# Kernel tuning notes

Measured on AMD Instinct MI355X. Metric: run time of the kernel, lower is better.

The kernel has to match this reference:

```python
import jax, jax.numpy as jnp
import numpy as np

B, N, F_IN = 4, 8000, 3          # batch, electrons per event, (x,y,z) features
HID, S, T = 128, 1024, 1024      # MLP hidden, n_sensors, waveform_ticks
INV_SQRT_2PI = 0.3989422804


def _mlp(x, W1, b1, W2, b2):
    h = jax.nn.relu(x @ W1 + b1)
    return h @ W2 + b2


def setup_inputs() -> dict:
    key = jax.random.key(0)
    ks = jax.random.split(key, 12)
    simulator_input = jax.random.normal(ks[0], (B, N, F_IN), dtype=jnp.float32)
    # z positions in tick units, spread across the waveform
    z_positions = jax.random.uniform(ks[1], (B, N), dtype=jnp.float32) * (T - 1)
    mask = jnp.ones((B, N, 1), dtype=jnp.float32)
    s1 = 1.0 / np.sqrt(F_IN)
    s2 = 1.0 / np.sqrt(HID)
    Wp1 = jax.random.normal(ks[2], (F_IN, HID), dtype=jnp.float32) * s1
    bp1 = jnp.zeros((HID,), dtype=jnp.float32)
    Wp2 = jax.random.normal(ks[3], (HID, S), dtype=jnp.float32) * s2
    bp2 = jnp.zeros((S,), dtype=jnp.float32)
    Wa1 = jax.random.normal(ks[4], (F_IN, HID), dtype=jnp.float32) * s1
    ba1 = jnp.zeros((HID,), dtype=jnp.float32)
    Wa2 = jax.random.normal(ks[5], (HID, S), dtype=jnp.float32) * s2
    ba2 = jnp.zeros((S,), dtype=jnp.float32)
    nn_bin_sigma = 5.0 * jnp.ones((1,), dtype=jnp.float32)  # self.variable init
    return dict(simulator_input=simulator_input, z_positions=z_positions, mask=mask,
                Wp1=Wp1, bp1=bp1, Wp2=Wp2, bp2=bp2,
                Wa1=Wa1, ba1=ba1, Wa2=Wa2, ba2=ba2,
                nn_bin_sigma=nn_bin_sigma)


def reference(simulator_input, z_positions, mask,
              Wp1, bp1, Wp2, bp2, Wa1, ba1, Wa2, ba2, nn_bin_sigma):
    # sensor response per electron: sigmoid(prob MLP) * amp MLP * mask  -> [B,N,S]
    sensor_probs = jax.nn.sigmoid(_mlp(simulator_input, Wp1, bp1, Wp2, bp2))
    el_light_amp = _mlp(simulator_input, Wa1, ba1, Wa2, ba2)
    response_of_sensors = el_light_amp * sensor_probs * mask

    # Gaussian binning kernel over waveform ticks: [B,N,T]
    ticks = jnp.arange(T, dtype=simulator_input.dtype)          # linspace(0, T-1, T)
    sigma = nn_bin_sigma[0]
    diff = ticks[None, None, :] - z_positions[:, :, None]
    exp_values = jnp.exp(-(diff ** 2) / (2.0 * sigma ** 2)) * (INV_SQRT_2PI / jnp.sqrt(sigma ** 2))

    # per-batch waveforms = sensor_response.T @ exp_values -> [B,S,T]; then sum over batch
    waveforms = jnp.einsum('bns,bnt->st', response_of_sensors, exp_values)
    return waveforms  # [S, T]
```

## Files before the change

kernel.cpp:

```cpp
#include <hip/hip_runtime.h>


#define BN_E   32000
#define NBLK   125
#define HIDW   128
#define S_DIM  1024
#define T_DIM  1024
#define NBKT   16
#define KSPL   4
#define MAXPAD (BN_E + NBKT * 31)
#define MAXCG  ((MAXPAD + 31) / 32)
#define INV_SQRT_2PI 0.3989422804f

typedef __attribute__((ext_vector_type(8))) unsigned short u16x8;
typedef __attribute__((ext_vector_type(8))) __bf16         bf16x8;
typedef __attribute__((ext_vector_type(4))) float          f32x4;

static __device__ __forceinline__ unsigned short f2bf(float f) {
    union { float f; unsigned int u; } v; v.f = f;
    unsigned int r = v.u + 0x7FFFu + ((v.u >> 16) & 1u);
    return (unsigned short)(r >> 16);
}

static __device__ __forceinline__ f32x4 mfma16(u16x8 a, u16x8 b, f32x4 c) {
    return __builtin_amdgcn_mfma_f32_16x16x32_bf16(
        __builtin_bit_cast(bf16x8, a), __builtin_bit_cast(bf16x8, b), c, 0, 0, 0);
}

static __device__ __forceinline__ int bucket_of(float z) {
    int b = (int)floorf((z - 31.f) * (1.f / 64.f));
    return min(max(b, 0), NBKT - 1);
}

__global__ __launch_bounds__(256) void k_count(const float* __restrict__ z,
                                               int* __restrict__ bc,
                                               float* __restrict__ out) {
    int bx = blockIdx.x;
    if (bx >= NBLK) {
        int idx = (bx - NBLK) * 256 + threadIdx.x;
        ((f32x4*)out)[idx] = (f32x4){0.f, 0.f, 0.f, 0.f};
        return;
    }
    __shared__ int h[NBKT];
    if (threadIdx.x < NBKT) h[threadIdx.x] = 0;
    __syncthreads();
    int e = bx * 256 + threadIdx.x;
    atomicAdd(&h[bucket_of(z[e])], 1);
    __syncthreads();
    if (threadIdx.x < NBKT) bc[bx * NBKT + threadIdx.x] = h[threadIdx.x];
}

__global__ __launch_bounds__(256) void k_fillscan(const float* __restrict__ z,
                                                  const int* __restrict__ bc,
                                                  int* __restrict__ meta,
                                                  int* __restrict__ list) {
    __shared__ int part[16][16];
    __shared__ int segoff[16][16];
    __shared__ int cntL[NBKT], pstartL[NBKT], baseL[NBKT], h[NBKT];
    int t = threadIdx.x, b = t & 15, seg = t >> 4;
    int v[8]; int sum = 0;
#pragma unroll
    for (int i = 0; i < 8; ++i) {
        int blk = seg * 8 + i;
        v[i] = (blk < NBLK) ? bc[blk * NBKT + b] : 0;
        sum += v[i];
    }
    part[seg][b] = sum;
    if (t < NBKT) h[t] = 0;
    __syncthreads();
    if (t < NBKT) {
        int run = 0;
        for (int s = 0; s < 16; ++s) { segoff[s][t] = run; run += part[s][t]; }
        cntL[t] = run;
    }
    __syncthreads();
    if (t == 0) {
        int s = 0;
        for (int i = 0; i < NBKT; ++i) {
            pstartL[i] = s;
            s += ((cntL[i] + 31) >> 5) << 5;
        }
        if (blockIdx.x == 0) {
            for (int i = 0; i < NBKT; ++i) { meta[i] = cntL[i]; meta[32 + i] = pstartL[i]; }
            meta[48] = s;
        }
    }
    __syncthreads();
    if (t < NBKT) {
        int me = blockIdx.x;
        int run = segoff[me >> 3][t];
        for (int k = 0; k < (me & 7); ++k)
            run += bc[((me >> 3) * 8 + k) * NBKT + t];
        baseL[t] = pstartL[t] + run;
    }
    __syncthreads();
    int e = blockIdx.x * 256 + t;
    int b2 = bucket_of(z[e]);
    int r = atomicAdd(&h[b2], 1);
    list[baseL[b2] + r] = e;
}

__global__ __launch_bounds__(256) void k_prep(
    const float* __restrict__ x, const float* __restrict__ zg,
    const float* __restrict__ maskg, const float* __restrict__ sigp,
    const float* __restrict__ Wp1, const float* __restrict__ bp1,
    const float* __restrict__ Wa1, const float* __restrict__ ba1,
    const float* __restrict__ Wp2, const float* __restrict__ Wa2,
    const int* __restrict__ meta, const int* __restrict__ list,
    unsigned short* __restrict__ HpS, unsigned short* __restrict__ HaS,
    unsigned short* __restrict__ GT,
    unsigned short* __restrict__ WfP, unsigned short* __restrict__ WfA) {
    int bx = blockIdx.x;
    if (bx < MAXCG) {
        int pos0 = bx * 32;
        if (pos0 >= meta[48]) return;
        int b = 15;
        while (meta[32 + b] > pos0) --b;
        int tb = b * 64, cnt = meta[b], pstart = meta[32 + b];
        int tid = threadIdx.x;

        __shared__ float W1L[1024];
        __shared__ float zzL[32], cmL[32];
        if (tid < 96)                        ((float4*)W1L)[tid]              = ((const float4*)Wp1)[tid];
        else if (tid < 128)                  ((float4*)(W1L + 384))[tid - 96] = ((const float4*)bp1)[tid - 96];
        else if (tid < 224)                  ((float4*)(W1L + 512))[tid - 128]= ((const float4*)Wa1)[tid - 128];
        else                                 ((float4*)(W1L + 896))[tid - 224]= ((const float4*)ba1)[tid - 224];
        if (tid < 32) {
            int pos = pos0 + tid;
            bool real = (pos - pstart) < cnt;
            int ev = real ? list[pos] : 0;
            float sigma = sigp[0];
            zzL[tid] = real ? zg[ev] : 0.f;
            cmL[tid] = real ? (INV_SQRT_2PI / sigma) * maskg[ev] : 0.f;
        }
        __syncthreads();

        {
            int e_l = tid >> 3, part = tid & 7;
            int pos = pos0 + e_l;
            bool real = (pos - pstart) < cnt;
            int ev = real ? list[pos] : 0;
            float x0 = 0.f, x1 = 0.f, x2 = 0.f;
            if (real) { x0 = x[ev * 3]; x1 = x[ev * 3 + 1]; x2 = x[ev * 3 + 2]; }
            unsigned short hp[16], ha[16];
#pragma unroll
            for (int i = 0; i < 16; ++i) {
                int j = part * 16 + i;
                float hv = x0 * W1L[j] + x1 * W1L[128 + j] + x2 * W1L[256 + j] + W1L[384 + j];
                float av = x0 * W1L[512 + j] + x1 * W1L[640 + j] + x2 * W1L[768 + j] + W1L[896 + j];
                hp[i] = real ? f2bf(fmaxf(hv, 0.f)) : (unsigned short)0;
                ha[i] = real ? f2bf(fmaxf(av, 0.f)) : (unsigned short)0;
            }
#pragma unroll
            for (int h2 = 0; h2 < 2; ++h2) {
                int k0 = part * 16 + h2 * 8;
                int u = ((k0 >> 5) * 4 + ((k0 >> 3) & 3)) * 32 + e_l;
                *(uint4*)&HpS[(size_t)bx * 4096 + u * 8] = ((uint4*)hp)[h2];
                *(uint4*)&HaS[(size_t)bx * 4096 + u * 8] = ((uint4*)ha)[h2];
            }
        }

        {
            float sigma = sigp[0];
            float nis2 = -1.f / (2.f * sigma * sigma);
#pragma unroll
            for (int uu = 0; uu < 2; ++uu) {
                int u = tid * 2 + uu;
                int n8 = u >> 6, q = (u >> 4) & 3, c = u & 15;
                float tt = (float)(tb + n8 * 16 + c);
                unsigned short g8[8];
#pragma unroll
                for (int j = 0; j < 8; ++j) {
                    int e = q * 8 + j;
                    float d = tt - zzL[e];
                    g8[j] = f2bf(cmL[e] * __expf(d * d * nis2));
                }
                *(uint4*)&GT[(size_t)bx * 4096 + u * 8] = *(uint4*)g8;
            }
        }
    } else {
        int bid = bx - MAXCG;
        const float* src = (bid & 64) ? Wa2 : Wp2;
        unsigned short* dst = (bid & 64) ? WfA : WfP;
        int rem = bid & 63;
        int kq = rem >> 2;
        int s  = (rem & 3) * 256 + threadIdx.x;
        int ks = kq >> 2, q = kq & 3;
        unsigned short fr[8];
#pragma unroll
        for (int j = 0; j < 8; ++j)
            fr[j] = f2bf(src[(ks * 32 + q * 8 + j) * S_DIM + s]);
        ((u16x8*)dst)[kq * S_DIM + s] = *(u16x8*)fr;
    }
}

__global__ __launch_bounds__(256, 4) void k_main(
    const unsigned short* __restrict__ HpS, const unsigned short* __restrict__ HaS,
    const unsigned short* __restrict__ WfP, const unsigned short* __restrict__ WfA,
    const float* __restrict__ bp2, const float* __restrict__ ba2,
    const int* __restrict__ meta, const unsigned short* __restrict__ GT,
    float* __restrict__ out) {

    const int bk     = blockIdx.x / KSPL;
    const int kspl   = blockIdx.x % KSPL;
    const int s0     = blockIdx.y * 64;
    const int tb     = bk * 64;
    const int cnt    = meta[bk];
    const int pstart = meta[32 + bk];
    const int nch    = (cnt + 31) >> 5;
    const int per    = (nch + KSPL - 1) / KSPL;
    const int c0     = kspl * per;
    const int c1     = min(nch, c0 + per);
    if (c0 >= c1) return;

    const int tid = threadIdx.x;
    const int w = tid >> 6, l = tid & 63, q = l >> 4, c = l & 15;

    __shared__ __align__(16) uint4 HpL[512];
    __shared__ __align__(16) uint4 HaL[512];
    __shared__ __align__(16) unsigned short RspL[64 * 40];

    const u16x8* WfPv = (const u16x8*)WfP;
    const u16x8* WfAv = (const u16x8*)WfA;
    const int sg = s0 + w * 16 + c;
    u16x8 wP[4], wA[4];
#pragma unroll
    for (int ks = 0; ks < 4; ++ks) {
        wP[ks] = WfPv[(ks * 4 + q) * S_DIM + sg];
        wA[ks] = WfAv[(ks * 4 + q) * S_DIM + sg];
    }
    const float bp2v = bp2[sg];
    const float ba2v = ba2[sg];

    const f32x4 z4 = { 0.f, 0.f, 0.f, 0.f };
    f32x4 acc2[8];
#pragma unroll
    for (int n8 = 0; n8 < 8; ++n8) acc2[n8] = z4;

    const uint4* Hp4 = (const uint4*)HpS;
    const uint4* Ha4 = (const uint4*)HaS;
    const int cgBase = pstart >> 5;
    const u16x8* StHp = (const u16x8*)HpL;
    const u16x8* StHa = (const u16x8*)HaL;

    size_t cb = (size_t)(cgBase + c0) * 512;
    uint4 p0 = Hp4[cb + tid], p1 = Hp4[cb + 256 + tid];
    uint4 a0 = Ha4[cb + tid], a1 = Ha4[cb + 256 + tid];

    for (int ci = c0; ci < c1; ++ci) {
        __syncthreads();
        HpL[tid] = p0; HpL[256 + tid] = p1;
        HaL[tid] = a0; HaL[256 + tid] = a1;
        __syncthreads();

        int nc = min(ci + 1, c1 - 1);
        cb = (size_t)(cgBase + nc) * 512;
        p0 = Hp4[cb + tid]; p1 = Hp4[cb + 256 + tid];
        a0 = Ha4[cb + tid]; a1 = Ha4[cb + 256 + tid];

        const unsigned short* gt = GT + (size_t)(cgBase + ci) * 4096;
        u16x8 bfr[8];
#pragma unroll
        for (int n8 = 0; n8 < 8; ++n8)
            bfr[n8] = *(const u16x8*)&gt[((n8 * 4 + q) * 16 + c) * 8];

        f32x4 aP[2], aA[2];
#pragma unroll
        for (int m = 0; m < 2; ++m) { aP[m] = z4; aA[m] = z4; }
#pragma unroll
        for (int ks = 0; ks < 4; ++ks) {
            u16x8 hp0 = StHp[(ks * 4 + q) * 32 + c];
            u16x8 hp1 = StHp[(ks * 4 + q) * 32 + c + 16];
            u16x8 ha0 = StHa[(ks * 4 + q) * 32 + c];
            u16x8 ha1 = StHa[(ks * 4 + q) * 32 + c + 16];
            aP[0] = mfma16(hp0, wP[ks], aP[0]);
            aP[1] = mfma16(hp1, wP[ks], aP[1]);
            aA[0] = mfma16(ha0, wA[ks], aA[0]);
            aA[1] = mfma16(ha1, wA[ks], aA[1]);
        }

#pragma unroll
        for (int m = 0; m < 2; ++m) {
            f32x4 p = aP[m], a = aA[m];
            unsigned long long pk = 0;
#pragma unroll
            for (int r = 0; r < 4; ++r) {
                float pr = p[r] + bp2v;
                float ar = a[r] + ba2v;
                float sg2 = __builtin_amdgcn_rcpf(1.f + __expf(-pr));
                pk |= (unsigned long long)f2bf(sg2 * ar) << (16 * r);
            }
            int sl = w * 16 + c;
            int e0 = m * 16 + q * 4;
            *(unsigned long long*)&RspL[sl * 40 + e0] = pk;
        }

        u16x8 afr = *(const u16x8*)&RspL[(w * 16 + c) * 40 + q * 8];
#pragma unroll
        for (int n8 = 0; n8 < 8; ++n8)
            acc2[n8] = mfma16(afr, bfr[n8], acc2[n8]);
    }

#pragma unroll
    for (int n8 = 0; n8 < 8; ++n8) {
        int t = tb + n8 * 16 + c;
        if (t < T_DIM) {
            int srow = s0 + w * 16 + q * 4;
#pragma unroll
            for (int r = 0; r < 4; ++r)
                atomicAdd(&out[(srow + r) * T_DIM + t], acc2[n8][r]);
        }
    }
}


extern "C" void kernel_launch(void* const* d_in, const int* in_sizes, int n_in,
                              void* d_out, int out_size, void* d_ws, size_t ws_size,
                              hipStream_t stream) {
    const float* x    = (const float*)d_in[0];
    const float* zp   = (const float*)d_in[1];
    const float* mask = (const float*)d_in[2];
    const float* Wp1  = (const float*)d_in[3];
    const float* bp1  = (const float*)d_in[4];
    const float* Wp2  = (const float*)d_in[5];
    const float* bp2  = (const float*)d_in[6];
    const float* Wa1  = (const float*)d_in[7];
    const float* ba1  = (const float*)d_in[8];
    const float* Wa2  = (const float*)d_in[9];
    const float* ba2  = (const float*)d_in[10];
    const float* sig  = (const float*)d_in[11];

    char* ws = (char*)d_ws;
    unsigned short* HpS  = (unsigned short*)(ws);
    unsigned short* HaS  = (unsigned short*)(ws + 8323072);
    unsigned short* WfP  = (unsigned short*)(ws + 16646144);
    unsigned short* WfA  = (unsigned short*)(ws + 16908288);
    int*            meta = (int*)(ws + 17170432);
    int*            list = (int*)(ws + 17170688);
    int*            bc   = (int*)(ws + 17300736);
    unsigned short* GT   = (unsigned short*)(ws + 17308736);

    k_count<<<NBLK + 1024, 256, 0, stream>>>(zp, bc, (float*)d_out);
    k_fillscan<<<NBLK, 256, 0, stream>>>(zp, bc, meta, list);
    k_prep<<<MAXCG + 128, 256, 0, stream>>>(x, zp, mask, sig,
                                            Wp1, bp1, Wa1, ba1, Wp2, Wa2,
                                            meta, list, HpS, HaS, GT, WfP, WfA);
    k_main<<<dim3(NBKT * KSPL, 16, 1), 256, 0, stream>>>(
        HpS, HaS, WfP, WfA, bp2, ba2, meta, GT, (float*)d_out);
}
```

Baseline: 153.3 us.

## Replace output atomics with partial-sum buffers and a separate reduce kernel

k_main no longer does atomicAdd into a zeroed output. Each block writes plain stores into one of eight 4 MB partial slabs, chosen by k-split and bucket parity, and a new k_reduce kernel sums the slabs into the output. The zero-fill that k_count used to do is removed. This drops atomic contention and the zero-init pass, but adds about 32 MB of partial writes plus a reduce pass that reads them back, and one more kernel launch. Blocks with no work now also store zeros.

```diff
diff --git a/kernel.cpp b/kernel.cpp
--- a/kernel.cpp
+++ b/kernel.cpp
@@ -33,21 +33,14 @@
 }
 
 __global__ __launch_bounds__(256) void k_count(const float* __restrict__ z,
-                                               int* __restrict__ bc,
-                                               float* __restrict__ out) {
-    int bx = blockIdx.x;
-    if (bx >= NBLK) {
-        int idx = (bx - NBLK) * 256 + threadIdx.x;
-        ((f32x4*)out)[idx] = (f32x4){0.f, 0.f, 0.f, 0.f};
-        return;
-    }
+                                               int* __restrict__ bc) {
     __shared__ int h[NBKT];
     if (threadIdx.x < NBKT) h[threadIdx.x] = 0;
     __syncthreads();
-    int e = bx * 256 + threadIdx.x;
+    int e = blockIdx.x * 256 + threadIdx.x;
     atomicAdd(&h[bucket_of(z[e])], 1);
     __syncthreads();
-    if (threadIdx.x < NBKT) bc[bx * NBKT + threadIdx.x] = h[threadIdx.x];
+    if (threadIdx.x < NBKT) bc[blockIdx.x * NBKT + threadIdx.x] = h[threadIdx.x];
 }
 
 __global__ __launch_bounds__(256) void k_fillscan(const float* __restrict__ z,
@@ -199,7 +192,7 @@
     const unsigned short* __restrict__ WfP, const unsigned short* __restrict__ WfA,
     const float* __restrict__ bp2, const float* __restrict__ ba2,
     const int* __restrict__ meta, const unsigned short* __restrict__ GT,
-    float* __restrict__ out) {
+    float* __restrict__ Acc) {
 
     const int bk     = blockIdx.x / KSPL;
     const int kspl   = blockIdx.x % KSPL;
@@ -211,7 +204,6 @@
     const int per    = (nch + KSPL - 1) / KSPL;
     const int c0     = kspl * per;
     const int c1     = min(nch, c0 + per);
-    if (c0 >= c1) return;
 
     const int tid = threadIdx.x;
     const int w = tid >> 6, l = tid & 63, q = l >> 4, c = l & 15;
@@ -220,87 +212,90 @@
     __shared__ __align__(16) uint4 HaL[512];
     __shared__ __align__(16) unsigned short RspL[64 * 40];
 
-    const u16x8* WfPv = (const u16x8*)WfP;
-    const u16x8* WfAv = (const u16x8*)WfA;
-    const int sg = s0 + w * 16 + c;
-    u16x8 wP[4], wA[4];
-#pragma unroll
-    for (int ks = 0; ks < 4; ++ks) {
-        wP[ks] = WfPv[(ks * 4 + q) * S_DIM + sg];
-        wA[ks] = WfAv[(ks * 4 + q) * S_DIM + sg];
-    }
-    const float bp2v = bp2[sg];
-    const float ba2v = ba2[sg];
-
     const f32x4 z4 = { 0.f, 0.f, 0.f, 0.f };
     f32x4 acc2[8];
 #pragma unroll
     for (int n8 = 0; n8 < 8; ++n8) acc2[n8] = z4;
 
-    const uint4* Hp4 = (const uint4*)HpS;
-    const uint4* Ha4 = (const uint4*)HaS;
-    const int cgBase = pstart >> 5;
-    const u16x8* StHp = (const u16x8*)HpL;
-    const u16x8* StHa = (const u16x8*)HaL;
-
-    size_t cb = (size_t)(cgBase + c0) * 512;
-    uint4 p0 = Hp4[cb + tid], p1 = Hp4[cb + 256 + tid];
-    uint4 a0 = Ha4[cb + tid], a1 = Ha4[cb + 256 + tid];
-
-    for (int ci = c0; ci < c1; ++ci) {
-        __syncthreads();
-        HpL[tid] = p0; HpL[256 + tid] = p1;
-        HaL[tid] = a0; HaL[256 + tid] = a1;
-        __syncthreads();
-
-        int nc = min(ci + 1, c1 - 1);
-        cb = (size_t)(cgBase + nc) * 512;
-        p0 = Hp4[cb + tid]; p1 = Hp4[cb + 256 + tid];
-        a0 = Ha4[cb + tid]; a1 = Ha4[cb + 256 + tid];
-
-        const unsigned short* gt = GT + (size_t)(cgBase + ci) * 4096;
-        u16x8 bfr[8];
-#pragma unroll
-        for (int n8 = 0; n8 < 8; ++n8)
-            bfr[n8] = *(const u16x8*)&gt[((n8 * 4 + q) * 16 + c) * 8];
-
-        f32x4 aP[2], aA[2];
-#pragma unroll
-        for (int m = 0; m < 2; ++m) { aP[m] = z4; aA[m] = z4; }
+    if (c0 < c1) {
+        const u16x8* WfPv = (const u16x8*)WfP;
+        const u16x8* WfAv = (const u16x8*)WfA;
+        const int sg = s0 + w * 16 + c;
+        u16x8 wP[4], wA[4];
 #pragma unroll
         for (int ks = 0; ks < 4; ++ks) {
-            u16x8 hp0 = StHp[(ks * 4 + q) * 32 + c];
-            u16x8 hp1 = StHp[(ks * 4 + q) * 32 + c + 16];
-            u16x8 ha0 = StHa[(ks * 4 + q) * 32 + c];
-            u16x8 ha1 = StHa[(ks * 4 + q) * 32 + c + 16];
-            aP[0] = mfma16(hp0, wP[ks], aP[0]);
-            aP[1] = mfma16(hp1, wP[ks], aP[1]);
-            aA[0] = mfma16(ha0, wA[ks], aA[0]);
-            aA[1] = mfma16(ha1, wA[ks], aA[1]);
-        }
-
-#pragma unroll
-        for (int m = 0; m < 2; ++m) {
-            f32x4 p = aP[m], a = aA[m];
-            unsigned long long pk = 0;
-#pragma unroll
-            for (int r = 0; r < 4; ++r) {
-                float pr = p[r] + bp2v;
-                float ar = a[r] + ba2v;
-                float sg2 = __builtin_amdgcn_rcpf(1.f + __expf(-pr));
-                pk |= (unsigned long long)f2bf(sg2 * ar) << (16 * r);
-            }
-            int sl = w * 16 + c;
-            int e0 = m * 16 + q * 4;
-            *(unsigned long long*)&RspL[sl * 40 + e0] = pk;
-        }
-
-        u16x8 afr = *(const u16x8*)&RspL[(w * 16 + c) * 40 + q * 8];
-#pragma unroll
-        for (int n8 = 0; n8 < 8; ++n8)
-            acc2[n8] = mfma16(afr, bfr[n8], acc2[n8]);
-    }
-
+            wP[ks] = WfPv[(ks * 4 + q) * S_DIM + sg];
+            wA[ks] = WfAv[(ks * 4 + q) * S_DIM + sg];
+        }
+        const float bp2v = bp2[sg];
+        const float ba2v = ba2[sg];
+
+        const uint4* Hp4 = (const uint4*)HpS;
+        const uint4* Ha4 = (const uint4*)HaS;
+        const int cgBase = pstart >> 5;
+        const u16x8* StHp = (const u16x8*)HpL;
+        const u16x8* StHa = (const u16x8*)HaL;
+
+        size_t cb = (size_t)(cgBase + c0) * 512;
+        uint4 p0 = Hp4[cb + tid], p1 = Hp4[cb + 256 + tid];
+        uint4 a0 = Ha4[cb + tid], a1 = Ha4[cb + 256 + tid];
+
+        for (int ci = c0; ci < c1; ++ci) {
+            __syncthreads();
+            HpL[tid] = p0; HpL[256 + tid] = p1;
+            HaL[tid] = a0; HaL[256 + tid] = a1;
+            __syncthreads();
+
+            int nc = min(ci + 1, c1 - 1);
+            cb = (size_t)(cgBase + nc) * 512;
+            p0 = Hp4[cb + tid]; p1 = Hp4[cb + 256 + tid];
+            a0 = Ha4[cb + tid]; a1 = Ha4[cb + 256 + tid];
+
+            const unsigned short* gt = GT + (size_t)(cgBase + ci) * 4096;
+            u16x8 bfr[8];
+#pragma unroll
+            for (int n8 = 0; n8 < 8; ++n8)
+                bfr[n8] = *(const u16x8*)&gt[((n8 * 4 + q) * 16 + c) * 8];
+
+            f32x4 aP[2], aA[2];
+#pragma unroll
+            for (int m = 0; m < 2; ++m) { aP[m] = z4; aA[m] = z4; }
+#pragma unroll
+            for (int ks = 0; ks < 4; ++ks) {
+                u16x8 hp0 = StHp[(ks * 4 + q) * 32 + c];
+                u16x8 hp1 = StHp[(ks * 4 + q) * 32 + c + 16];
+                u16x8 ha0 = StHa[(ks * 4 + q) * 32 + c];
+                u16x8 ha1 = StHa[(ks * 4 + q) * 32 + c + 16];
+                aP[0] = mfma16(hp0, wP[ks], aP[0]);
+                aP[1] = mfma16(hp1, wP[ks], aP[1]);
+                aA[0] = mfma16(ha0, wA[ks], aA[0]);
+                aA[1] = mfma16(ha1, wA[ks], aA[1]);
+            }
+
+#pragma unroll
+            for (int m = 0; m < 2; ++m) {
+                f32x4 p = aP[m], a = aA[m];
+                unsigned long long pk = 0;
+#pragma unroll
+                for (int r = 0; r < 4; ++r) {
+                    float pr = p[r] + bp2v;
+                    float ar = a[r] + ba2v;
+                    float sg2 = __builtin_amdgcn_rcpf(1.f + __expf(-pr));
+                    pk |= (unsigned long long)f2bf(sg2 * ar) << (16 * r);
+                }
+                int sl = w * 16 + c;
+                int e0 = m * 16 + q * 4;
+                *(unsigned long long*)&RspL[sl * 40 + e0] = pk;
+            }
+
+            u16x8 afr = *(const u16x8*)&RspL[(w * 16 + c) * 40 + q * 8];
+#pragma unroll
+            for (int n8 = 0; n8 < 8; ++n8)
+                acc2[n8] = mfma16(afr, bfr[n8], acc2[n8]);
+        }
+    }
+
+    float* dst = Acc + ((size_t)(kspl * 2 + (bk & 1)) << 20);
 #pragma unroll
     for (int n8 = 0; n8 < 8; ++n8) {
         int t = tb + n8 * 16 + c;
@@ -308,9 +303,21 @@
             int srow = s0 + w * 16 + q * 4;
 #pragma unroll
             for (int r = 0; r < 4; ++r)
-                atomicAdd(&out[(srow + r) * T_DIM + t], acc2[n8][r]);
-        }
-    }
+                dst[(srow + r) * T_DIM + t] = acc2[n8][r];
+        }
+    }
+}
+
+__global__ __launch_bounds__(256) void k_reduce(const float* __restrict__ Acc,
+                                                float* __restrict__ out) {
+    int i = blockIdx.x * 256 + threadIdx.x;
+    int t4 = (i & 255) * 4;
+    const f32x4* A = (const f32x4*)Acc;
+    const int SL = 1 << 18;
+    f32x4 s = A[i] + A[2 * SL + i] + A[4 * SL + i] + A[6 * SL + i];
+    if (t4 >= 64)
+        s += A[SL + i] + A[3 * SL + i] + A[5 * SL + i] + A[7 * SL + i];
+    ((f32x4*)out)[i] = s;
 }
 
 
@@ -339,12 +346,14 @@
     int*            list = (int*)(ws + 17170688);
     int*            bc   = (int*)(ws + 17300736);
     unsigned short* GT   = (unsigned short*)(ws + 17308736);
-
-    k_count<<<NBLK + 1024, 256, 0, stream>>>(zp, bc, (float*)d_out);
+    float*          Acc  = (float*)(ws + 25631808);
+
+    k_count<<<NBLK, 256, 0, stream>>>(zp, bc);
     k_fillscan<<<NBLK, 256, 0, stream>>>(zp, bc, meta, list);
     k_prep<<<MAXCG + 128, 256, 0, stream>>>(x, zp, mask, sig,
                                             Wp1, bp1, Wa1, ba1, Wp2, Wa2,
                                             meta, list, HpS, HaS, GT, WfP, WfA);
     k_main<<<dim3(NBKT * KSPL, 16, 1), 256, 0, stream>>>(
-        HpS, HaS, WfP, WfA, bp2, ba2, meta, GT, (float*)d_out);
-}
+        HpS, HaS, WfP, WfA, bp2, ba2, meta, GT, Acc);
+    k_reduce<<<1024, 256, 0, stream>>>(Acc, (float*)d_out);
+}
```

After: 153.9 us. No clear change (+0.4%).

## Fuse count/MLP prep into one kernel and compute Gaussian tiles inside main kernel

Applied to the files above, without the earlier changes.

Merges the bucket-count, first-layer MLP, weight conversion and output zeroing into one pre kernel. The hidden activations are now stored in unsorted event order, and k_main gathers them through the sorted list. The Gaussian binning tile is computed on the fly in k_main into shared memory instead of being precomputed to global memory. This removes one kernel launch and the global write and read of the Gaussian tiles. In exchange, k_main does redundant exp work across its 16 sensor-block y tiles, does indirect gathers, and adds an extra barrier per chunk.

```diff
diff --git a/kernel.cpp b/kernel.cpp
--- a/kernel.cpp
+++ b/kernel.cpp
@@ -9,8 +9,12 @@
 #define NBKT   16
 #define KSPL   4
 #define MAXPAD (BN_E + NBKT * 31)
-#define MAXCG  ((MAXPAD + 31) / 32)
 #define INV_SQRT_2PI 0.3989422804f
+
+#define HB 16000
+#define CB NBLK
+#define WB 128
+#define ZB 1024
 
 typedef __attribute__((ext_vector_type(8))) unsigned short u16x8;
 typedef __attribute__((ext_vector_type(8))) __bf16         bf16x8;
@@ -32,22 +36,48 @@
     return min(max(b, 0), NBKT - 1);
 }
 
-__global__ __launch_bounds__(256) void k_count(const float* __restrict__ z,
-                                               int* __restrict__ bc,
-                                               float* __restrict__ out) {
-    int bx = blockIdx.x;
-    if (bx >= NBLK) {
-        int idx = (bx - NBLK) * 256 + threadIdx.x;
+__global__ __launch_bounds__(256) void k_pre(
+    const float* __restrict__ x, const float* __restrict__ zp,
+    const float* __restrict__ Wp1, const float* __restrict__ bp1,
+    const float* __restrict__ Wa1, const float* __restrict__ ba1,
+    const float* __restrict__ Wp2, const float* __restrict__ Wa2,
+    unsigned short* __restrict__ HpU, unsigned short* __restrict__ HaU,
+    unsigned short* __restrict__ WfP, unsigned short* __restrict__ WfA,
+    int* __restrict__ bc, float* __restrict__ out) {
+    __shared__ int h[NBKT];
+    int bx = blockIdx.x, tid = threadIdx.x;
+    if (bx < HB) {
+        int e = bx * 2 + (tid >> 7);
+        int j = tid & 127;
+        float x0 = x[e * 3 + 0], x1 = x[e * 3 + 1], x2 = x[e * 3 + 2];
+        float hp = x0 * Wp1[j] + x1 * Wp1[HIDW + j] + x2 * Wp1[2 * HIDW + j] + bp1[j];
+        float ha = x0 * Wa1[j] + x1 * Wa1[HIDW + j] + x2 * Wa1[2 * HIDW + j] + ba1[j];
+        HpU[e * HIDW + j] = f2bf(fmaxf(hp, 0.f));
+        HaU[e * HIDW + j] = f2bf(fmaxf(ha, 0.f));
+    } else if (bx < HB + CB) {
+        if (tid < NBKT) h[tid] = 0;
+        __syncthreads();
+        int e = (bx - HB) * 256 + tid;
+        atomicAdd(&h[bucket_of(zp[e])], 1);
+        __syncthreads();
+        if (tid < NBKT) bc[(bx - HB) * NBKT + tid] = h[tid];
+    } else if (bx < HB + CB + WB) {
+        int bid = bx - HB - CB;
+        const float* src = (bid & 64) ? Wa2 : Wp2;
+        unsigned short* dst = (bid & 64) ? WfA : WfP;
+        int rem = bid & 63;
+        int kq = rem >> 2;
+        int s  = (rem & 3) * 256 + tid;
+        int ks = kq >> 2, q = kq & 3;
+        unsigned short fr[8];
+#pragma unroll
+        for (int j = 0; j < 8; ++j)
+            fr[j] = f2bf(src[(ks * 32 + q * 8 + j) * S_DIM + s]);
+        ((u16x8*)dst)[kq * S_DIM + s] = *(u16x8*)fr;
+    } else {
+        int idx = (bx - HB - CB - WB) * 256 + tid;
         ((f32x4*)out)[idx] = (f32x4){0.f, 0.f, 0.f, 0.f};
-        return;
-    }
-    __shared__ int h[NBKT];
-    if (threadIdx.x < NBKT) h[threadIdx.x] = 0;
-    __syncthreads();
-    int e = bx * 256 + threadIdx.x;
-    atomicAdd(&h[bucket_of(z[e])], 1);
-    __syncthreads();
-    if (threadIdx.x < NBKT) bc[bx * NBKT + threadIdx.x] = h[threadIdx.x];
+    }
 }
 
 __global__ __launch_bounds__(256) void k_fillscan(const float* __restrict__ z,
@@ -100,105 +130,13 @@
     list[baseL[b2] + r] = e;
 }
 
-__global__ __launch_bounds__(256) void k_prep(
-    const float* __restrict__ x, const float* __restrict__ zg,
-    const float* __restrict__ maskg, const float* __restrict__ sigp,
-    const float* __restrict__ Wp1, const float* __restrict__ bp1,
-    const float* __restrict__ Wa1, const float* __restrict__ ba1,
-    const float* __restrict__ Wp2, const float* __restrict__ Wa2,
-    const int* __restrict__ meta, const int* __restrict__ list,
-    unsigned short* __restrict__ HpS, unsigned short* __restrict__ HaS,
-    unsigned short* __restrict__ GT,
-    unsigned short* __restrict__ WfP, unsigned short* __restrict__ WfA) {
-    int bx = blockIdx.x;
-    if (bx < MAXCG) {
-        int pos0 = bx * 32;
-        if (pos0 >= meta[48]) return;
-        int b = 15;
-        while (meta[32 + b] > pos0) --b;
-        int tb = b * 64, cnt = meta[b], pstart = meta[32 + b];
-        int tid = threadIdx.x;
-
-        __shared__ float W1L[1024];
-        __shared__ float zzL[32], cmL[32];
-        if (tid < 96)                        ((float4*)W1L)[tid]              = ((const float4*)Wp1)[tid];
-        else if (tid < 128)                  ((float4*)(W1L + 384))[tid - 96] = ((const float4*)bp1)[tid - 96];
-        else if (tid < 224)                  ((float4*)(W1L + 512))[tid - 128]= ((const float4*)Wa1)[tid - 128];
-        else                                 ((float4*)(W1L + 896))[tid - 224]= ((const float4*)ba1)[tid - 224];
-        if (tid < 32) {
-            int pos = pos0 + tid;
-            bool real = (pos - pstart) < cnt;
-            int ev = real ? list[pos] : 0;
-            float sigma = sigp[0];
-            zzL[tid] = real ? zg[ev] : 0.f;
-            cmL[tid] = real ? (INV_SQRT_2PI / sigma) * maskg[ev] : 0.f;
-        }
-        __syncthreads();
-
-        {
-            int e_l = tid >> 3, part = tid & 7;
-            int pos = pos0 + e_l;
-            bool real = (pos - pstart) < cnt;
-            int ev = real ? list[pos] : 0;
-            float x0 = 0.f, x1 = 0.f, x2 = 0.f;
-            if (real) { x0 = x[ev * 3]; x1 = x[ev * 3 + 1]; x2 = x[ev * 3 + 2]; }
-            unsigned short hp[16], ha[16];
-#pragma unroll
-            for (int i = 0; i < 16; ++i) {
-                int j = part * 16 + i;
-                float hv = x0 * W1L[j] + x1 * W1L[128 + j] + x2 * W1L[256 + j] + W1L[384 + j];
-                float av = x0 * W1L[512 + j] + x1 * W1L[640 + j] + x2 * W1L[768 + j] + W1L[896 + j];
-                hp[i] = real ? f2bf(fmaxf(hv, 0.f)) : (unsigned short)0;
-                ha[i] = real ? f2bf(fmaxf(av, 0.f)) : (unsigned short)0;
-            }
-#pragma unroll
-            for (int h2 = 0; h2 < 2; ++h2) {
-                int k0 = part * 16 + h2 * 8;
-                int u = ((k0 >> 5) * 4 + ((k0 >> 3) & 3)) * 32 + e_l;
-                *(uint4*)&HpS[(size_t)bx * 4096 + u * 8] = ((uint4*)hp)[h2];
-                *(uint4*)&HaS[(size_t)bx * 4096 + u * 8] = ((uint4*)ha)[h2];
-            }
-        }
-
-        {
-            float sigma = sigp[0];
-            float nis2 = -1.f / (2.f * sigma * sigma);
-#pragma unroll
-            for (int uu = 0; uu < 2; ++uu) {
-                int u = tid * 2 + uu;
-                int n8 = u >> 6, q = (u >> 4) & 3, c = u & 15;
-                float tt = (float)(tb + n8 * 16 + c);
-                unsigned short g8[8];
-#pragma unroll
-                for (int j = 0; j < 8; ++j) {
-                    int e = q * 8 + j;
-                    float d = tt - zzL[e];
-                    g8[j] = f2bf(cmL[e] * __expf(d * d * nis2));
-                }
-                *(uint4*)&GT[(size_t)bx * 4096 + u * 8] = *(uint4*)g8;
-            }
-        }
-    } else {
-        int bid = bx - MAXCG;
-        const float* src = (bid & 64) ? Wa2 : Wp2;
-        unsigned short* dst = (bid & 64) ? WfA : WfP;
-        int rem = bid & 63;
-        int kq = rem >> 2;
-        int s  = (rem & 3) * 256 + threadIdx.x;
-        int ks = kq >> 2, q = kq & 3;
-        unsigned short fr[8];
-#pragma unroll
-        for (int j = 0; j < 8; ++j)
-            fr[j] = f2bf(src[(ks * 32 + q * 8 + j) * S_DIM + s]);
-        ((u16x8*)dst)[kq * S_DIM + s] = *(u16x8*)fr;
-    }
-}
-
 __global__ __launch_bounds__(256, 4) void k_main(
-    const unsigned short* __restrict__ HpS, const unsigned short* __restrict__ HaS,
+    const unsigned short* __restrict__ HpU, const unsigned short* __restrict__ HaU,
     const unsigned short* __restrict__ WfP, const unsigned short* __restrict__ WfA,
     const float* __restrict__ bp2, const float* __restrict__ ba2,
-    const int* __restrict__ meta, const unsigned short* __restrict__ GT,
+    const float* __restrict__ zp, const float* __restrict__ maskg,
+    const float* __restrict__ sigp,
+    const int* __restrict__ meta, const int* __restrict__ list,
     float* __restrict__ out) {
 
     const int bk     = blockIdx.x / KSPL;
@@ -216,9 +154,11 @@
     const int tid = threadIdx.x;
     const int w = tid >> 6, l = tid & 63, q = l >> 4, c = l & 15;
 
-    __shared__ __align__(16) uint4 HpL[512];
-    __shared__ __align__(16) uint4 HaL[512];
+    __shared__ __align__(16) uint4 HpL[16 * 34];
+    __shared__ __align__(16) uint4 HaL[16 * 34];
+    __shared__ __align__(16) uint4 GL[512];
     __shared__ __align__(16) unsigned short RspL[64 * 40];
+    __shared__ float zzL[32], cmL[32];
 
     const u16x8* WfPv = (const u16x8*)WfP;
     const u16x8* WfAv = (const u16x8*)WfA;
@@ -232,47 +172,81 @@
     const float bp2v = bp2[sg];
     const float ba2v = ba2[sg];
 
+    const float sigma = sigp[0];
+    const float coef  = INV_SQRT_2PI / sigma;
+    const float nis2  = -1.f / (2.f * sigma * sigma);
+
     const f32x4 z4 = { 0.f, 0.f, 0.f, 0.f };
     f32x4 acc2[8];
 #pragma unroll
     for (int n8 = 0; n8 < 8; ++n8) acc2[n8] = z4;
 
-    const uint4* Hp4 = (const uint4*)HpS;
-    const uint4* Ha4 = (const uint4*)HaS;
-    const int cgBase = pstart >> 5;
-    const u16x8* StHp = (const u16x8*)HpL;
-    const u16x8* StHa = (const u16x8*)HaL;
-
-    size_t cb = (size_t)(cgBase + c0) * 512;
-    uint4 p0 = Hp4[cb + tid], p1 = Hp4[cb + 256 + tid];
-    uint4 a0 = Ha4[cb + tid], a1 = Ha4[cb + 256 + tid];
+    const uint4* Hp4 = (const uint4*)HpU;
+    const uint4* Ha4 = (const uint4*)HaU;
+    const u16x8* HpV = (const u16x8*)HpL;
+    const u16x8* HaV = (const u16x8*)HaL;
+    const u16x8* GLv = (const u16x8*)GL;
+
+    const int e_l = tid >> 3, kq0 = tid & 7;
+
+    int evS = (c0 * 32 + e_l < cnt) ? list[pstart + c0 * 32 + e_l] : 0;
+    uint4 p0 = Hp4[evS * 16 + kq0], p1 = Hp4[evS * 16 + kq0 + 8];
+    uint4 a0 = Ha4[evS * 16 + kq0], a1 = Ha4[evS * 16 + kq0 + 8];
+    float zzn = 0.f, cmn = 0.f;
+    if (tid < 32) {
+        bool r2 = (c0 * 32 + tid) < cnt;
+        int ev2 = r2 ? list[pstart + c0 * 32 + tid] : 0;
+        zzn = r2 ? zp[ev2] : 0.f;
+        cmn = r2 ? coef * maskg[ev2] : 0.f;
+    }
 
     for (int ci = c0; ci < c1; ++ci) {
         __syncthreads();
-        HpL[tid] = p0; HpL[256 + tid] = p1;
-        HaL[tid] = a0; HaL[256 + tid] = a1;
-        __syncthreads();
+        HpL[kq0 * 34 + e_l] = p0; HpL[(kq0 + 8) * 34 + e_l] = p1;
+        HaL[kq0 * 34 + e_l] = a0; HaL[(kq0 + 8) * 34 + e_l] = a1;
+        if (tid < 32) { zzL[tid] = zzn; cmL[tid] = cmn; }
+        __syncthreads();
+
+        {
+            int q4 = (tid >> 4) & 3;
+            float zr[8], cr[8];
+#pragma unroll
+            for (int j = 0; j < 8; ++j) { zr[j] = zzL[q4 * 8 + j]; cr[j] = cmL[q4 * 8 + j]; }
+#pragma unroll
+            for (int uu = 0; uu < 2; ++uu) {
+                int u = tid + uu * 256;
+                int n8 = u >> 6, cc = u & 15;
+                float tt = (float)(tb + n8 * 16 + cc);
+                unsigned short g8[8];
+#pragma unroll
+                for (int j = 0; j < 8; ++j) {
+                    float d = tt - zr[j];
+                    g8[j] = f2bf(cr[j] * __expf(d * d * nis2));
+                }
+                GL[u] = *(uint4*)g8;
+            }
+        }
 
         int nc = min(ci + 1, c1 - 1);
-        cb = (size_t)(cgBase + nc) * 512;
-        p0 = Hp4[cb + tid]; p1 = Hp4[cb + 256 + tid];
-        a0 = Ha4[cb + tid]; a1 = Ha4[cb + 256 + tid];
-
-        const unsigned short* gt = GT + (size_t)(cgBase + ci) * 4096;
-        u16x8 bfr[8];
-#pragma unroll
-        for (int n8 = 0; n8 < 8; ++n8)
-            bfr[n8] = *(const u16x8*)&gt[((n8 * 4 + q) * 16 + c) * 8];
+        int evSn = (nc * 32 + e_l < cnt) ? list[pstart + nc * 32 + e_l] : 0;
+        p0 = Hp4[evSn * 16 + kq0]; p1 = Hp4[evSn * 16 + kq0 + 8];
+        a0 = Ha4[evSn * 16 + kq0]; a1 = Ha4[evSn * 16 + kq0 + 8];
+        if (tid < 32) {
+            bool r2 = (nc * 32 + tid) < cnt;
+            int ev2 = r2 ? list[pstart + nc * 32 + tid] : 0;
+            zzn = r2 ? zp[ev2] : 0.f;
+            cmn = r2 ? coef * maskg[ev2] : 0.f;
+        }
 
         f32x4 aP[2], aA[2];
 #pragma unroll
         for (int m = 0; m < 2; ++m) { aP[m] = z4; aA[m] = z4; }
 #pragma unroll
         for (int ks = 0; ks < 4; ++ks) {
-            u16x8 hp0 = StHp[(ks * 4 + q) * 32 + c];
-            u16x8 hp1 = StHp[(ks * 4 + q) * 32 + c + 16];
-            u16x8 ha0 = StHa[(ks * 4 + q) * 32 + c];
-            u16x8 ha1 = StHa[(ks * 4 + q) * 32 + c + 16];
+            u16x8 hp0 = HpV[(ks * 4 + q) * 34 + c];
+            u16x8 hp1 = HpV[(ks * 4 + q) * 34 + c + 16];
+            u16x8 ha0 = HaV[(ks * 4 + q) * 34 + c];
+            u16x8 ha1 = HaV[(ks * 4 + q) * 34 + c + 16];
             aP[0] = mfma16(hp0, wP[ks], aP[0]);
             aP[1] = mfma16(hp1, wP[ks], aP[1]);
             aA[0] = mfma16(ha0, wA[ks], aA[0]);
@@ -295,10 +269,12 @@
             *(unsigned long long*)&RspL[sl * 40 + e0] = pk;
         }
 
+        __syncthreads();
+
         u16x8 afr = *(const u16x8*)&RspL[(w * 16 + c) * 40 + q * 8];
 #pragma unroll
         for (int n8 = 0; n8 < 8; ++n8)
-            acc2[n8] = mfma16(afr, bfr[n8], acc2[n8]);
+            acc2[n8] = mfma16(afr, GLv[(n8 * 4 + q) * 16 + c], acc2[n8]);
     }
 
 #pragma unroll
@@ -331,20 +307,17 @@
     const float* sig  = (const float*)d_in[11];
 
     char* ws = (char*)d_ws;
-    unsigned short* HpS  = (unsigned short*)(ws);
-    unsigned short* HaS  = (unsigned short*)(ws + 8323072);
-    unsigned short* WfP  = (unsigned short*)(ws + 16646144);
-    unsigned short* WfA  = (unsigned short*)(ws + 16908288);
-    int*            meta = (int*)(ws + 17170432);
-    int*            list = (int*)(ws + 17170688);
-    int*            bc   = (int*)(ws + 17300736);
-    unsigned short* GT   = (unsigned short*)(ws + 17308736);
-
-    k_count<<<NBLK + 1024, 256, 0, stream>>>(zp, bc, (float*)d_out);
+    unsigned short* HpU  = (unsigned short*)(ws);
+    unsigned short* HaU  = (unsigned short*)(ws + 8192000);
+    unsigned short* WfP  = (unsigned short*)(ws + 16384000);
+    unsigned short* WfA  = (unsigned short*)(ws + 16646144);
+    int*            meta = (int*)(ws + 16908288);
+    int*            list = (int*)(ws + 16908544);
+    int*            bc   = (int*)(ws + 17038592);
+
+    k_pre<<<HB + CB + WB + ZB, 256, 0, stream>>>(
+        x, zp, Wp1, bp1, Wa1, ba1, Wp2, Wa2, HpU, HaU, WfP, WfA, bc, (float*)d_out);
     k_fillscan<<<NBLK, 256, 0, stream>>>(zp, bc, meta, list);
-    k_prep<<<MAXCG + 128, 256, 0, stream>>>(x, zp, mask, sig,
-                                            Wp1, bp1, Wa1, ba1, Wp2, Wa2,
-                                            meta, list, HpS, HaS, GT, WfP, WfA);
     k_main<<<dim3(NBKT * KSPL, 16, 1), 256, 0, stream>>>(
-        HpS, HaS, WfP, WfA, bp2, ba2, meta, GT, (float*)d_out);
-}
+        HpU, HaU, WfP, WfA, bp2, ba2, zp, mask, sig, meta, list, (float*)d_out);
+}
```

After: 175.7 us. 1.15x slower.
